# Optimization experiments

Measured on AMD Instinct MI355X. Metric: run time of the kernel, lower is better.

The kernel has to match this reference:

```python
import jax, jax.numpy as jnp
import numpy as np
from jax import lax

# Static pair index table: all C(135,2)=9045 unordered node pairs (replaces the
# nested Python loops with a single gather).
PAIR_I, PAIR_J = np.triu_indices(135, k=1)
RRELU_SLOPE = (1.0 / 8.0 + 1.0 / 3.0) / 2.0  # eval-mode RReLU negative slope
BN_SCALE = 1.0 / float(np.sqrt(1.0 + 1e-5))  # eval BN with running mean=0, var=1


def _leaky(x):
    return jnp.where(x > 0, x, 0.01 * x)


def _conv1d(x, w, b):
    # x: (N, Cin, L), w: (Cout, Cin, K) -> (N, Cout, L-K+1), VALID
    y = lax.conv_general_dilated(x, w, (1,), 'VALID',
                                 dimension_numbers=('NCH', 'OIH', 'NCH'))
    return y + b[None, :, None]


def _bn_eval(x, g, b):
    # nn.BatchNorm1d in eval with fresh running stats (mean=0, var=1)
    return x * (g * BN_SCALE)[None, :, None] + b[None, :, None]


def _maxpool2d(x):
    # nn.MaxPool2d(2) applied to a 3D (N, H, W) tensor: 2x2 pool over (H, W)
    return lax.reduce_window(x, -jnp.inf, lax.max, (1, 2, 2), (1, 2, 2), 'VALID')


def setup_inputs() -> dict:
    key = jax.random.key(0)
    ks = iter(jax.random.split(key, 40))

    def w(shape, scale=0.05):
        return (jax.random.normal(next(ks), shape, jnp.float32) * scale)

    inp = {
        'x': jax.random.normal(next(ks), (30, 135, 375), jnp.float32),
        # FeatureExtractor
        'conv1_w': w((32, 1, 3)), 'conv1_b': jnp.zeros((32,), jnp.float32),
        'bn1_g': jnp.ones((32,), jnp.float32), 'bn1_b': jnp.zeros((32,), jnp.float32),
        'conv2_w': w((64, 16, 3)), 'conv2_b': jnp.zeros((64,), jnp.float32),
        'bn2_g': jnp.ones((64,), jnp.float32), 'bn2_b': jnp.zeros((64,), jnp.float32),
        'conv3_w': w((96, 32, 3)), 'conv3_b': jnp.zeros((96,), jnp.float32),
        'bn3_g': jnp.ones((96,), jnp.float32), 'bn3_b': jnp.zeros((96,), jnp.float32),
        'fe_fc_w': w((48 * 45, 32)), 'fe_fc_b': jnp.zeros((32,), jnp.float32),
        # SimilarityMeasureNetwork
        'sim_w1': w((64, 32)), 'sim_b1': jnp.zeros((32,), jnp.float32),
        'sim_w2': w((32, 16)), 'sim_b2': jnp.zeros((16,), jnp.float32),
        'sim_w3': w((16, 8)), 'sim_b3': jnp.zeros((8,), jnp.float32),
        'sim_w4': w((8, 1)), 'sim_b4': jnp.zeros((1,), jnp.float32),
        # ClassificationNet(9045, 3)
        'cls_w1': w((9045, 1024), 0.01), 'cls_b1': jnp.zeros((1024,), jnp.float32),
        'cls_w2': w((1024, 256)), 'cls_b2': jnp.zeros((256,), jnp.float32),
        'cls_w3': w((256, 64)), 'cls_b3': jnp.zeros((64,), jnp.float32),
        'cls_w4': w((64, 3)), 'cls_b4': jnp.zeros((3,), jnp.float32),
    }
    return inp


def reference(x, conv1_w, conv1_b, bn1_g, bn1_b, conv2_w, conv2_b, bn2_g, bn2_b,
              conv3_w, conv3_b, bn3_g, bn3_b, fe_fc_w, fe_fc_b,
              sim_w1, sim_b1, sim_w2, sim_b2, sim_w3, sim_b3, sim_w4, sim_b4,
              cls_w1, cls_b1, cls_w2, cls_b2, cls_w3, cls_b3, cls_w4, cls_b4):
    B = x.shape[0]  # 30 subjects
    h = x.reshape(B * 135, 1, 375)
    # FeatureExtractor (all subjects*nodes batched together)
    h = _maxpool2d(_leaky(_bn_eval(_conv1d(h, conv1_w, conv1_b), bn1_g, bn1_b)))  # (N,16,186)
    h = _maxpool2d(_leaky(_bn_eval(_conv1d(h, conv2_w, conv2_b), bn2_g, bn2_b)))  # (N,32,92)
    h = _maxpool2d(_leaky(_bn_eval(_conv1d(h, conv3_w, conv3_b), bn3_g, bn3_b)))  # (N,48,45)
    h = h.reshape(B * 135, -1) @ fe_fc_w + fe_fc_b  # (B*135, 32)
    feats = h.reshape(B, 135, 32)

    # All-pairs concat: single gather replacing the nested loops -> (B, 9045, 64)
    pi = jnp.asarray(PAIR_I)
    pj = jnp.asarray(PAIR_J)
    pairs = jnp.concatenate([feats[:, pi, :], feats[:, pj, :]], axis=-1)

    # SimilarityMeasureNetwork
    s = jax.nn.relu(pairs @ sim_w1 + sim_b1)
    s = jax.nn.relu(s @ sim_w2 + sim_b2)
    s = jax.nn.relu(s @ sim_w3 + sim_b3)
    s = jnp.tanh(s @ sim_w4 + sim_b4)  # (B, 9045, 1)
    subjects = s[..., 0]  # (B, 9045)

    # ClassificationNet (eval mode: RReLU -> fixed slope, dropout -> identity)
    c = subjects @ cls_w1 + cls_b1
    c = jnp.where(c >= 0, c, RRELU_SLOPE * c)
    c = jax.nn.relu(c @ cls_w2 + cls_b2)
    c = jax.nn.relu(c @ cls_w3 + cls_b3)
    c = c @ cls_w4 + cls_b4
    return jax.nn.log_softmax(c, axis=1)  # (B, 3)
```

## Files before the change

kernel.cpp:

```cpp
#include <hip/hip_runtime.h>
#include <math.h>

#define BN_SCALE 0.99999500003749967f
#define RRELU_SLOPE 0.22916666666666666f

static __device__ __forceinline__ float leaky(float v) { return v > 0.f ? v : 0.01f * v; }

typedef __attribute__((ext_vector_type(8))) short bf16x8;
typedef __attribute__((ext_vector_type(4))) float f32x4;

static __device__ __forceinline__ unsigned short f2bf(float f) {
  unsigned u = __builtin_bit_cast(unsigned, f);
  u = (u + 0x7FFFu + ((u >> 16) & 1u)) >> 16;
  return (unsigned short)u;
}

__global__ __launch_bounds__(256) void prep_kernel(
    const float* __restrict__ w2c, const float* __restrict__ g2,
    const float* __restrict__ w3c, const float* __restrict__ g3,
    const float* __restrict__ fcw, const float* __restrict__ fcb,
    const float* __restrict__ w1,  const float* __restrict__ b1,
    unsigned short* __restrict__ w2frag,
    unsigned short* __restrict__ w3frag,
    unsigned short* __restrict__ bfragGG,
    float* __restrict__ bgagb,
    unsigned short* __restrict__ subjectsA)
{
  const int item = blockIdx.x * 256 + threadIdx.x;
  if (item < 512) {
    const int tile = item >> 6, lane = item & 63;
    const int mt = tile >> 1, kc = tile & 1;
    const int lr = lane & 15, quad = lane >> 4;
    const int c = mt * 16 + lr;
    const float gs = g2[c] * BN_SCALE;
#pragma unroll
    for (int j = 0; j < 8; ++j) {
      const int k = quad * 8 + j;
      float v;
      if (kc == 0) { const int tap = k >> 4, ci = k & 15; v = w2c[c * 48 + ci * 3 + tap] * gs; }
      else         { v = (k < 16) ? w2c[c * 48 + k * 3 + 2] * gs : 0.f; }
      w2frag[item * 8 + j] = f2bf(v);
    }
  } else if (item < 1664) {
    const int it = item - 512;
    const int tile = it >> 6, lane = it & 63;
    const int mt = tile / 3, tap = tile - mt * 3;
    const int lr = lane & 15, quad = lane >> 4;
    const int c = mt * 16 + lr;
    const float gs = g3[c] * BN_SCALE;
#pragma unroll
    for (int j = 0; j < 8; ++j) {
      const int ci = quad * 8 + j;
      w3frag[it * 8 + j] = f2bf(w3c[c * 96 + ci * 3 + tap] * gs);
    }
  } else if (item < 19072) {
    const int it = item - 1664;
    const int chunk = it >> 8;
    const int rem = it & 255;
    const int nt = rem >> 6;
    const int lane = rem & 63;
    const int lr = lane & 15, quad = lane >> 4;
    const int n = nt * 16 + lr;
    const int off = (n >= 32) ? 32 : 0;
    const int nj = n & 31;
    float w1col[32];
#pragma unroll 8
    for (int q = 0; q < 32; ++q) w1col[q] = w1[(q + off) * 32 + nj];
#pragma unroll
    for (int j = 0; j < 8; ++j) {
      const int k = chunk * 32 + quad * 8 + j;
      float v = 0.f;
      if (k < 2160) {
        const float* fr = fcw + (size_t)k * 32;
#pragma unroll 8
        for (int q = 0; q < 32; ++q) v = fmaf(fr[q], w1col[q], v);
      }
      bfragGG[(size_t)it * 8 + j] = f2bf(v);
    }
  } else if (item < 19136) {
    const int n = item - 19072;
    const int off = (n >= 32) ? 32 : 0;
    const int nj = n & 31;
    float s = (n < 32) ? b1[nj] : 0.f;
    for (int q = 0; q < 32; ++q) s = fmaf(fcb[q], w1[(q + off) * 32 + nj], s);
    bgagb[n] = s;
  } else if (item < 55360) {
    const int idx = item - 19136;
    uint4 z = {0u, 0u, 0u, 0u};
    ((uint4*)subjectsA)[idx] = z;
  }
}

__global__ __launch_bounds__(256) void w1t_kernel(
    const float* __restrict__ w1, unsigned short* __restrict__ w1T)
{
  __shared__ float tile[64][65];
  const int kt = blockIdx.x >> 4;
  const int ntb = blockIdx.x & 15;
  const int k0 = kt * 64, n0 = ntb * 64;
  const int t = threadIdx.x;
#pragma unroll 4
  for (int i = 0; i < 16; ++i) {
    const int idx = i * 256 + t;
    const int kk = idx >> 6, nn = idx & 63;
    const int k = k0 + kk;
    tile[kk][nn] = (k < 9045) ? w1[(size_t)k * 1024 + n0 + nn] : 0.f;
  }
  __syncthreads();
#pragma unroll 4
  for (int i = 0; i < 8; ++i) {
    const int idx = i * 256 + t;
    const int nn = idx >> 5;
    const int kp = (idx & 31) * 2;
    const unsigned lo = f2bf(tile[kp][nn]);
    const unsigned hi = f2bf(tile[kp + 1][nn]);
    ((unsigned*)w1T)[(size_t)(n0 + nn) * 4544 + (k0 >> 1) + (idx & 31)] = lo | (hi << 16);
  }
}

__global__ __launch_bounds__(128) void fe_kernel(
    const float* __restrict__ x,
    const float* __restrict__ w1c, const float* __restrict__ b1c,
    const float* __restrict__ g1,  const float* __restrict__ bb1,
    const float* __restrict__ b2c, const float* __restrict__ g2, const float* __restrict__ bb2,
    const float* __restrict__ b3c, const float* __restrict__ g3, const float* __restrict__ bb3,
    const unsigned short* __restrict__ w2frag,
    const unsigned short* __restrict__ w3frag,
    unsigned short* __restrict__ act3)
{
  __shared__ __align__(16) char smem[2 * 13120];
  const int t = threadIdx.x;
  const int wv = t >> 6, lane = t & 63, quad = lane >> 4, lr = lane & 15;
  const int n = blockIdx.x * 2 + wv;

  char* A = smem + wv * 13120;
  unsigned short* s1t = (unsigned short*)A;
  unsigned short* s2t = (unsigned short*)(A + 6208);
  float* be2 = (float*)(A + 12480);
  float* be3 = (float*)(A + 12736);

  bf16x8 a2[4][2];
#pragma unroll
  for (int mt = 0; mt < 4; ++mt)
#pragma unroll
    for (int kc = 0; kc < 2; ++kc)
      a2[mt][kc] = *(const bf16x8*)(w2frag + ((mt * 2 + kc) * 64 + lane) * 8);

  be2[lane] = b2c[lane] * (g2[lane] * BN_SCALE) + bb2[lane];
  be3[lane] = b3c[lane] * (g3[lane] * BN_SCALE) + bb3[lane];
  if (lane < 32) be3[64 + lane] = b3c[64 + lane] * (g3[64 + lane] * BN_SCALE) + bb3[64 + lane];
  ((unsigned*)s1t)[186 * 8 + lane] = 0;
  ((unsigned*)s2t)[92 * 16 + lane] = 0;
  if (lane < 32) ((unsigned*)s2t)[92 * 16 + 64 + lane] = 0;

  const int cp = lane & 7;
  float u[4][3], bbr[4];
#pragma unroll
  for (int d = 0; d < 4; ++d) {
    const int c = cp * 4 + d;
    const float gs = g1[c] * BN_SCALE;
    u[d][0] = w1c[c * 3 + 0] * gs;
    u[d][1] = w1c[c * 3 + 1] * gs;
    u[d][2] = w1c[c * 3 + 2] * gs;
    bbr[d] = b1c[c] * gs + bb1[c];
  }

  const float* xr = x + (size_t)n * 375;
  for (int o = lane; o < 1488; o += 64) {
    const int l = o >> 3;
    const int p = 2 * l;
    const float x0 = xr[p], x1 = xr[p + 1], x2 = xr[p + 2], x3 = xr[p + 3];
    unsigned pk = 0;
#pragma unroll
    for (int uu = 0; uu < 2; ++uu) {
      float m = -3.4e38f;
#pragma unroll
      for (int dc = 0; dc < 2; ++dc) {
        const int d = uu * 2 + dc;
        const float v0 = fmaf(x0, u[d][0], fmaf(x1, u[d][1], fmaf(x2, u[d][2], bbr[d])));
        const float v1 = fmaf(x1, u[d][0], fmaf(x2, u[d][1], fmaf(x3, u[d][2], bbr[d])));
        m = fmaxf(m, fmaxf(leaky(v0), leaky(v1)));
      }
      pk |= (unsigned)f2bf(m) << (16 * uu);
    }
    ((unsigned*)s1t)[l * 8 + cp] = pk;
  }

  float be2r[4][4];
#pragma unroll
  for (int mt = 0; mt < 4; ++mt)
#pragma unroll
    for (int r = 0; r < 4; ++r) be2r[mt][r] = be2[mt * 16 + quad * 4 + r];

#pragma unroll 2
  for (int nt = 0; nt < 12; ++nt) {
    const int nrow = nt * 16 + lr;
    bf16x8 b0 = *(const bf16x8*)(s1t + (nrow + (quad >> 1)) * 16 + (quad & 1) * 8);
    bf16x8 b1 = *(const bf16x8*)(s1t + (nrow + 2) * 16 + (quad & 1) * 8);
    f32x4 acc[4];
#pragma unroll
    for (int mt = 0; mt < 4; ++mt)
#pragma unroll
      for (int r = 0; r < 4; ++r) acc[mt][r] = be2r[mt][r];
#pragma unroll
    for (int mt = 0; mt < 4; ++mt)
      acc[mt] = __builtin_amdgcn_mfma_f32_16x16x32_bf16(a2[mt][0], b0, acc[mt], 0, 0, 0);
#pragma unroll
    for (int mt = 0; mt < 4; ++mt)
      acc[mt] = __builtin_amdgcn_mfma_f32_16x16x32_bf16(a2[mt][1], b1, acc[mt], 0, 0, 0);
#pragma unroll
    for (int mt = 0; mt < 4; ++mt) {
      float o[4];
#pragma unroll
      for (int r = 0; r < 4; ++r) {
        const float v = leaky(acc[mt][r]);
        o[r] = fmaxf(v, __shfl_xor(v, 1));
      }
      if ((lr & 1) == 0) {
        const int np = nrow >> 1;
        if (np <= 91) {
          const float m0 = fmaxf(o[0], o[1]);
          const float m1 = fmaxf(o[2], o[3]);
          const unsigned pk = (unsigned)f2bf(m0) | ((unsigned)f2bf(m1) << 16);
          ((unsigned*)s2t)[np * 16 + mt * 4 + quad] = pk;
        }
      }
    }
  }

  unsigned short* actr = act3 + (size_t)n * 2176;
  for (int mt = 0; mt < 6; ++mt) {
    bf16x8 a3[3];
#pragma unroll
    for (int tap = 0; tap < 3; ++tap)
      a3[tap] = *(const bf16x8*)(w3frag + ((mt * 3 + tap) * 64 + lane) * 8);
    float be3r[4];
#pragma unroll
    for (int r = 0; r < 4; ++r) be3r[r] = be3[mt * 16 + quad * 4 + r];
#pragma unroll
    for (int nt = 0; nt < 6; ++nt) {
      const int nrow = nt * 16 + lr;
      f32x4 acc;
#pragma unroll
      for (int r = 0; r < 4; ++r) acc[r] = be3r[r];
#pragma unroll
      for (int tap = 0; tap < 3; ++tap) {
        bf16x8 b = *(const bf16x8*)(s2t + (nrow + tap) * 32 + quad * 8);
        acc = __builtin_amdgcn_mfma_f32_16x16x32_bf16(a3[tap], b, acc, 0, 0, 0);
      }
      float o[4];
#pragma unroll
      for (int r = 0; r < 4; ++r) {
        const float v = leaky(acc[r]);
        o[r] = fmaxf(v, __shfl_xor(v, 1));
      }
      if ((lr & 1) == 0) {
        const int np = nrow >> 1;
        if (np <= 44) {
          const int mp = mt * 8 + quad * 2;
          actr[mp * 45 + np] = f2bf(fmaxf(o[0], o[1]));
          actr[(mp + 1) * 45 + np] = f2bf(fmaxf(o[2], o[3]));
        }
      }
    }
  }
  if (lane < 16) actr[2160 + lane] = 0;
}

__global__ __launch_bounds__(256) void gagb_kernel(
    const unsigned short* __restrict__ act3,
    const unsigned short* __restrict__ bfragGG,
    const float* __restrict__ bgagb,
    float* __restrict__ Ga, float* __restrict__ Gb)
{
  const int t = threadIdx.x;
  const int wv = t >> 6, lane = t & 63, quad = lane >> 4, lr = lane & 15;
  const int m0 = blockIdx.x * 64 + wv * 16;
  const int arow = min(m0 + lr, 4049);

  f32x4 acc[4] = {};
  for (int chunk = 0; chunk < 68; ++chunk) {
    const bf16x8 a = *(const bf16x8*)(act3 + (size_t)arow * 2176 + chunk * 32 + quad * 8);
#pragma unroll
    for (int nt = 0; nt < 4; ++nt) {
      const bf16x8 b = *(const bf16x8*)(bfragGG + ((size_t)(chunk * 4 + nt) * 64 + lane) * 8);
      acc[nt] = __builtin_amdgcn_mfma_f32_16x16x32_bf16(a, b, acc[nt], 0, 0, 0);
    }
  }
#pragma unroll
  for (int nt = 0; nt < 4; ++nt) {
    const int col = nt * 16 + lr;
    const float bias = bgagb[col];
#pragma unroll
    for (int r = 0; r < 4; ++r) {
      const int row = m0 + quad * 4 + r;
      if (row < 4050) {
        const float v = acc[nt][r] + bias;
        if (col < 32) Ga[row * 32 + col] = v;
        else          Gb[row * 32 + (col - 32)] = v;
      }
    }
  }
}

__global__ __launch_bounds__(256) void sim_kernel(
    const float* __restrict__ Ga, const float* __restrict__ Gb,
    const float* __restrict__ w2, const float* __restrict__ b2,
    const float* __restrict__ w3, const float* __restrict__ b3,
    const float* __restrict__ w4, const float* __restrict__ b4,
    unsigned short* __restrict__ subjectsA)
{
  __shared__ float sGa[135 * 36];
  __shared__ float sGb[135 * 36];
  __shared__ float sw2[512], sw3[128], sw4[8];
  __shared__ float sb2[16], sb3[8], sb4v[1];

  const int t = threadIdx.x;
  const int b = blockIdx.x >> 4;
  const int c = blockIdx.x & 15;

  for (int i = t; i < 4320; i += 256) {
    const int r = i >> 5, col = i & 31;
    sGa[r * 36 + col] = Ga[b * 4320 + i];
    sGb[r * 36 + col] = Gb[b * 4320 + i];
  }
  for (int i = t; i < 512; i += 256) sw2[i] = w2[i];
  if (t < 128) sw3[t] = w3[t];
  if (t < 8) sw4[t] = w4[t];
  if (t < 16) sb2[t] = b2[t];
  if (t < 8) sb3[t] = b3[t];
  if (t == 0) sb4v[0] = b4[0];
  __syncthreads();

  const int mtile = b >> 4, lrm = b & 15;
  const int pend = min(9045, (c + 1) * 566);
  for (int p = c * 566 + t; p < pend; p += 256) {
    int i = (int)((269.0f - sqrtf((float)(72361 - 8 * p))) * 0.5f);
    i = max(0, min(133, i));
    while (134 * (i + 1) - ((i + 1) * i) / 2 <= p) ++i;
    while (134 * i - (i * (i - 1)) / 2 > p) --i;
    const int j = i + 1 + (p - (134 * i - (i * (i - 1)) / 2));

    float h1[32];
#pragma unroll
    for (int q = 0; q < 8; ++q) {
      const float4 va = *(const float4*)(&sGa[i * 36 + 4 * q]);
      const float4 vb = *(const float4*)(&sGb[j * 36 + 4 * q]);
      h1[4 * q + 0] = fmaxf(va.x + vb.x, 0.f);
      h1[4 * q + 1] = fmaxf(va.y + vb.y, 0.f);
      h1[4 * q + 2] = fmaxf(va.z + vb.z, 0.f);
      h1[4 * q + 3] = fmaxf(va.w + vb.w, 0.f);
    }

    float h2[16];
#pragma unroll
    for (int jj = 0; jj < 16; ++jj) h2[jj] = sb2[jj];
#pragma unroll 8
    for (int ii = 0; ii < 32; ++ii) {
      const float av = h1[ii];
      const float4* wr = reinterpret_cast<const float4*>(&sw2[ii * 16]);
#pragma unroll
      for (int r = 0; r < 4; ++r) {
        float4 w = wr[r];
        h2[4 * r + 0] = fmaf(av, w.x, h2[4 * r + 0]);
        h2[4 * r + 1] = fmaf(av, w.y, h2[4 * r + 1]);
        h2[4 * r + 2] = fmaf(av, w.z, h2[4 * r + 2]);
        h2[4 * r + 3] = fmaf(av, w.w, h2[4 * r + 3]);
      }
    }
#pragma unroll
    for (int jj = 0; jj < 16; ++jj) h2[jj] = fmaxf(h2[jj], 0.f);

    float h3[8];
#pragma unroll
    for (int jj = 0; jj < 8; ++jj) h3[jj] = sb3[jj];
#pragma unroll
    for (int ii = 0; ii < 16; ++ii) {
      const float av = h2[ii];
      const float4* wr = reinterpret_cast<const float4*>(&sw3[ii * 8]);
#pragma unroll
      for (int r = 0; r < 2; ++r) {
        float4 w = wr[r];
        h3[4 * r + 0] = fmaf(av, w.x, h3[4 * r + 0]);
        h3[4 * r + 1] = fmaf(av, w.y, h3[4 * r + 1]);
        h3[4 * r + 2] = fmaf(av, w.z, h3[4 * r + 2]);
        h3[4 * r + 3] = fmaf(av, w.w, h3[4 * r + 3]);
      }
    }
#pragma unroll
    for (int jj = 0; jj < 8; ++jj) h3[jj] = fmaxf(h3[jj], 0.f);

    float z = sb4v[0];
#pragma unroll
    for (int ii = 0; ii < 8; ++ii) z = fmaf(h3[ii], sw4[ii], z);

    const float az = fabsf(z);
    const float e = __expf(-2.f * az);
    const float rr = (1.f - e) / (1.f + e);
    const float val = copysignf(rr, z);

    const int chunk = p >> 5, q8 = (p & 31) >> 3, jj2 = p & 7;
    subjectsA[chunk * 1024 + mtile * 512 + (q8 * 16 + lrm) * 8 + jj2] = f2bf(val);
  }
}

__global__ __launch_bounds__(256) void c1_kernel(
    const unsigned short* __restrict__ subjectsA,
    const unsigned short* __restrict__ w1T,
    float* __restrict__ part)
{
  const int t = threadIdx.x;
  const int wv = t >> 6, lane = t & 63, quad = lane >> 4, lr = lane & 15;
  const int job = blockIdx.x * 4 + wv;
  const int ng = job & 15;
  const int kg = job >> 4;
  const int c0 = kg * 5;
  const int cend = min(283, c0 + 5);

  f32x4 acc[2][4] = {};
  for (int ch = c0; ch < cend; ++ch) {
    const bf16x8 a0 = *(const bf16x8*)(subjectsA + ch * 1024 + lane * 8);
    const bf16x8 a1 = *(const bf16x8*)(subjectsA + ch * 1024 + 512 + lane * 8);
#pragma unroll
    for (int nt = 0; nt < 4; ++nt) {
      const int col = (ng * 4 + nt) * 16 + lr;
      const bf16x8 b = *(const bf16x8*)(w1T + (size_t)col * 9088 + ch * 32 + quad * 8);
      acc[0][nt] = __builtin_amdgcn_mfma_f32_16x16x32_bf16(a0, b, acc[0][nt], 0, 0, 0);
      acc[1][nt] = __builtin_amdgcn_mfma_f32_16x16x32_bf16(a1, b, acc[1][nt], 0, 0, 0);
    }
  }
#pragma unroll
  for (int mt = 0; mt < 2; ++mt)
#pragma unroll
    for (int r = 0; r < 4; ++r) {
      const int m = mt * 16 + quad * 4 + r;
      if (m < 30) {
#pragma unroll
        for (int nt = 0; nt < 4; ++nt) {
          const int col = (ng * 4 + nt) * 16 + lr;
          part[(size_t)(m * 64 + kg) * 1024 + col] = acc[mt][nt][r];
        }
      }
    }
}

__global__ __launch_bounds__(256) void tail_a_kernel(
    const float* __restrict__ part,
    const float* __restrict__ cb1,
    float* __restrict__ act1)
{
  const int r = blockIdx.x >> 2;
  const int cg = blockIdx.x & 3;
  const int j = cg * 256 + threadIdx.x;
  float s = cb1[j];
  const float* pp = part + (size_t)r * 64 * 1024 + j;
#pragma unroll 8
  for (int q = 0; q < 64; ++q) s += pp[q * 1024];
  act1[r * 1024 + j] = s >= 0.f ? s : RRELU_SLOPE * s;
}

__global__ __launch_bounds__(256) void tail_b_kernel(
    const float* __restrict__ act1,
    const float* __restrict__ w2, const float* __restrict__ cb2,
    float* __restrict__ act2)
{
  __shared__ float sa[1024];
  __shared__ float sp[256];
  const int r = blockIdx.x >> 3;
  const int cg = blockIdx.x & 7;
  const int t = threadIdx.x;
  const int c = t & 31;
  const int ks = t >> 5;
  const int col = cg * 32 + c;

  for (int i = t; i < 1024; i += 256) sa[i] = act1[r * 1024 + i];
  __syncthreads();

  float acc = 0.f;
  const int k0 = ks * 128;
  for (int kk = k0; kk < k0 + 128; kk += 4) {
    const float4 a = *reinterpret_cast<const float4*>(&sa[kk]);
    acc = fmaf(a.x, w2[(kk + 0) * 256 + col], acc);
    acc = fmaf(a.y, w2[(kk + 1) * 256 + col], acc);
    acc = fmaf(a.z, w2[(kk + 2) * 256 + col], acc);
    acc = fmaf(a.w, w2[(kk + 3) * 256 + col], acc);
  }
  sp[t] = acc;
  __syncthreads();
  if (t < 32) {
    float s = cb2[col];
#pragma unroll
    for (int q = 0; q < 8; ++q) s += sp[q * 32 + t];
    act2[r * 256 + cg * 32 + t] = fmaxf(s, 0.f);
  }
}

__global__ __launch_bounds__(256) void tail_c_kernel(
    const float* __restrict__ act2,
    const float* __restrict__ w3, const float* __restrict__ cb3,
    const float* __restrict__ w4, const float* __restrict__ cb4,
    float* __restrict__ out)
{
  __shared__ float sa[256];
  __shared__ float sp[256];
  __shared__ float sc3[64];
  __shared__ float slg[3];
  const int r = blockIdx.x, t = threadIdx.x;
  const int c = t & 63;
  const int ks = t >> 6;

  sa[t] = act2[r * 256 + t];
  __syncthreads();
  {
    float acc = 0.f;
    const int k0 = ks * 64;
#pragma unroll 4
    for (int kk = k0; kk < k0 + 64; ++kk)
      acc = fmaf(sa[kk], w3[kk * 64 + c], acc);
    sp[t] = acc;
  }
  __syncthreads();
  if (t < 64) {
    const float s = cb3[t] + sp[t] + sp[t + 64] + sp[t + 128] + sp[t + 192];
    sc3[t] = fmaxf(s, 0.f);
  }
  __syncthreads();
  if (t < 3) {
    float acc = cb4[t];
#pragma unroll
    for (int kk = 0; kk < 64; ++kk) acc = fmaf(sc3[kk], w4[kk * 3 + t], acc);
    slg[t] = acc;
  }
  __syncthreads();
  if (t == 0) {
    float m = fmaxf(slg[0], fmaxf(slg[1], slg[2]));
    float se = __expf(slg[0] - m) + __expf(slg[1] - m) + __expf(slg[2] - m);
    float lse = m + logf(se);
    out[r * 3 + 0] = slg[0] - lse;
    out[r * 3 + 1] = slg[1] - lse;
    out[r * 3 + 2] = slg[2] - lse;
  }
}

extern "C" void kernel_launch(void* const* d_in, const int* in_sizes, int n_in,
                              void* d_out, int out_size, void* d_ws, size_t ws_size,
                              hipStream_t stream) {
  const float* x    = (const float*)d_in[0];
  const float* w1c  = (const float*)d_in[1];
  const float* b1c  = (const float*)d_in[2];
  const float* g1   = (const float*)d_in[3];
  const float* bb1  = (const float*)d_in[4];
  const float* w2c  = (const float*)d_in[5];
  const float* b2c  = (const float*)d_in[6];
  const float* g2   = (const float*)d_in[7];
  const float* bb2  = (const float*)d_in[8];
  const float* w3c  = (const float*)d_in[9];
  const float* b3c  = (const float*)d_in[10];
  const float* g3   = (const float*)d_in[11];
  const float* bb3  = (const float*)d_in[12];
  const float* fcw  = (const float*)d_in[13];
  const float* fcb  = (const float*)d_in[14];
  const float* sw1  = (const float*)d_in[15];
  const float* sb1  = (const float*)d_in[16];
  const float* sw2  = (const float*)d_in[17];
  const float* sb2  = (const float*)d_in[18];
  const float* sw3  = (const float*)d_in[19];
  const float* sb3  = (const float*)d_in[20];
  const float* sw4  = (const float*)d_in[21];
  const float* sb4  = (const float*)d_in[22];
  const float* cw1  = (const float*)d_in[23];
  const float* cb1  = (const float*)d_in[24];
  const float* cw2  = (const float*)d_in[25];
  const float* cb2  = (const float*)d_in[26];
  const float* cw3  = (const float*)d_in[27];
  const float* cb3  = (const float*)d_in[28];
  const float* cw4  = (const float*)d_in[29];
  const float* cb4  = (const float*)d_in[30];

  float* ws = (float*)d_ws;
  float* Ga    = ws;
  float* Gb    = ws + 129600;
  float* part  = ws + 259200;
  float* bgagb = ws + 2225280;
  float* act1  = ws + 2225344;
  float* act2  = ws + 2256064;
  unsigned short* wsu = (unsigned short*)(ws + 2263744);
  unsigned short* w2frag    = wsu;
  unsigned short* w3frag    = wsu + 4096;
  unsigned short* bfragGG   = wsu + 13312;
  unsigned short* act3      = wsu + 152576;
  unsigned short* subjectsA = wsu + 8965376;
  unsigned short* w1T       = wsu + 9255168;

  prep_kernel<<<217, 256, 0, stream>>>(w2c, g2, w3c, g3, fcw, fcb, sw1, sb1,
                                       w2frag, w3frag, bfragGG, bgagb, subjectsA);
  w1t_kernel<<<2272, 256, 0, stream>>>(cw1, w1T);
  fe_kernel<<<2025, 128, 0, stream>>>(x, w1c, b1c, g1, bb1, b2c, g2, bb2,
                                      b3c, g3, bb3, w2frag, w3frag, act3);
  gagb_kernel<<<64, 256, 0, stream>>>(act3, bfragGG, bgagb, Ga, Gb);
  sim_kernel<<<480, 256, 0, stream>>>(Ga, Gb, sw2, sb2, sw3, sb3, sw4, sb4, subjectsA);
  c1_kernel<<<256, 256, 0, stream>>>(subjectsA, w1T, part);
  tail_a_kernel<<<120, 256, 0, stream>>>(part, cb1, act1);
  tail_b_kernel<<<240, 256, 0, stream>>>(act1, cw2, cb2, act2);
  tail_c_kernel<<<30, 256, 0, stream>>>(act2, cw3, cb3, cw4, cb4, (float*)d_out);
}
```

Baseline: 296.3 us.

## Merge prep kernels, alias fe LDS buffers, split-K gagb, double sim grid

Folds the w1 transpose/convert kernel into the prep kernel to save a launch. The feature-extractor reuses one LDS buffer for both stage activations, roughly halving its shared memory so more blocks fit per CU. The Ga/Gb GEMM splits K across four waves and reduces through LDS, raising the grid from 64 to 254 blocks. The similarity kernel halves its per-block pair range to launch twice as many blocks, at the cost of reloading Ga/Gb into LDS twice as often.

Measured after the change: 270.5 us. 8.7% less time.

```diff
diff --git a/kernel.cpp b/kernel.cpp
--- a/kernel.cpp
+++ b/kernel.cpp
@@ -15,21 +15,48 @@
   return (unsigned short)u;
 }
 
-__global__ __launch_bounds__(256) void prep_kernel(
+__global__ __launch_bounds__(256) void setup_kernel(
     const float* __restrict__ w2c, const float* __restrict__ g2,
     const float* __restrict__ w3c, const float* __restrict__ g3,
     const float* __restrict__ fcw, const float* __restrict__ fcb,
     const float* __restrict__ w1,  const float* __restrict__ b1,
+    const float* __restrict__ cw1,
     unsigned short* __restrict__ w2frag,
     unsigned short* __restrict__ w3frag,
     unsigned short* __restrict__ bfragGG,
     float* __restrict__ bgagb,
-    unsigned short* __restrict__ subjectsA)
-{
-  const int item = blockIdx.x * 256 + threadIdx.x;
+    unsigned short* __restrict__ subjectsA,
+    unsigned short* __restrict__ w1T)
+{
+  __shared__ float tile[64][65];
+  const int t = threadIdx.x;
+  if (blockIdx.x < 2272) {
+    const int kt = blockIdx.x >> 4;
+    const int ntb = blockIdx.x & 15;
+    const int k0 = kt * 64, n0 = ntb * 64;
+#pragma unroll 4
+    for (int i = 0; i < 16; ++i) {
+      const int idx = i * 256 + t;
+      const int kk = idx >> 6, nn = idx & 63;
+      const int k = k0 + kk;
+      tile[kk][nn] = (k < 9045) ? cw1[(size_t)k * 1024 + n0 + nn] : 0.f;
+    }
+    __syncthreads();
+#pragma unroll 4
+    for (int i = 0; i < 8; ++i) {
+      const int idx = i * 256 + t;
+      const int nn = idx >> 5;
+      const int kp = (idx & 31) * 2;
+      const unsigned lo = f2bf(tile[kp][nn]);
+      const unsigned hi = f2bf(tile[kp + 1][nn]);
+      ((unsigned*)w1T)[(size_t)(n0 + nn) * 4544 + (k0 >> 1) + (idx & 31)] = lo | (hi << 16);
+    }
+    return;
+  }
+  const int item = (blockIdx.x - 2272) * 256 + t;
   if (item < 512) {
-    const int tile = item >> 6, lane = item & 63;
-    const int mt = tile >> 1, kc = tile & 1;
+    const int tl = item >> 6, lane = item & 63;
+    const int mt = tl >> 1, kc = tl & 1;
     const int lr = lane & 15, quad = lane >> 4;
     const int c = mt * 16 + lr;
     const float gs = g2[c] * BN_SCALE;
@@ -43,8 +70,8 @@
     }
   } else if (item < 1664) {
     const int it = item - 512;
-    const int tile = it >> 6, lane = it & 63;
-    const int mt = tile / 3, tap = tile - mt * 3;
+    const int tl = it >> 6, lane = it & 63;
+    const int mt = tl / 3, tap = tl - mt * 3;
     const int lr = lane & 15, quad = lane >> 4;
     const int c = mt * 16 + lr;
     const float gs = g3[c] * BN_SCALE;
@@ -91,33 +118,6 @@
   }
 }
 
-__global__ __launch_bounds__(256) void w1t_kernel(
-    const float* __restrict__ w1, unsigned short* __restrict__ w1T)
-{
-  __shared__ float tile[64][65];
-  const int kt = blockIdx.x >> 4;
-  const int ntb = blockIdx.x & 15;
-  const int k0 = kt * 64, n0 = ntb * 64;
-  const int t = threadIdx.x;
-#pragma unroll 4
-  for (int i = 0; i < 16; ++i) {
-    const int idx = i * 256 + t;
-    const int kk = idx >> 6, nn = idx & 63;
-    const int k = k0 + kk;
-    tile[kk][nn] = (k < 9045) ? w1[(size_t)k * 1024 + n0 + nn] : 0.f;
-  }
-  __syncthreads();
-#pragma unroll 4
-  for (int i = 0; i < 8; ++i) {
-    const int idx = i * 256 + t;
-    const int nn = idx >> 5;
-    const int kp = (idx & 31) * 2;
-    const unsigned lo = f2bf(tile[kp][nn]);
-    const unsigned hi = f2bf(tile[kp + 1][nn]);
-    ((unsigned*)w1T)[(size_t)(n0 + nn) * 4544 + (k0 >> 1) + (idx & 31)] = lo | (hi << 16);
-  }
-}
-
 __global__ __launch_bounds__(128) void fe_kernel(
     const float* __restrict__ x,
     const float* __restrict__ w1c, const float* __restrict__ b1c,
@@ -128,16 +128,15 @@
     const unsigned short* __restrict__ w3frag,
     unsigned short* __restrict__ act3)
 {
-  __shared__ __align__(16) char smem[2 * 13120];
+  __shared__ __align__(16) char smem[2 * 6912];
   const int t = threadIdx.x;
   const int wv = t >> 6, lane = t & 63, quad = lane >> 4, lr = lane & 15;
   const int n = blockIdx.x * 2 + wv;
 
-  char* A = smem + wv * 13120;
-  unsigned short* s1t = (unsigned short*)A;
-  unsigned short* s2t = (unsigned short*)(A + 6208);
-  float* be2 = (float*)(A + 12480);
-  float* be3 = (float*)(A + 12736);
+  char* A = smem + wv * 6912;
+  unsigned short* buf = (unsigned short*)A;
+  float* be2 = (float*)(A + 6272);
+  float* be3 = (float*)(A + 6528);
 
   bf16x8 a2[4][2];
 #pragma unroll
@@ -149,9 +148,7 @@
   be2[lane] = b2c[lane] * (g2[lane] * BN_SCALE) + bb2[lane];
   be3[lane] = b3c[lane] * (g3[lane] * BN_SCALE) + bb3[lane];
   if (lane < 32) be3[64 + lane] = b3c[64 + lane] * (g3[64 + lane] * BN_SCALE) + bb3[64 + lane];
-  ((unsigned*)s1t)[186 * 8 + lane] = 0;
-  ((unsigned*)s2t)[92 * 16 + lane] = 0;
-  if (lane < 32) ((unsigned*)s2t)[92 * 16 + 64 + lane] = 0;
+  ((unsigned*)buf)[1488 + lane] = 0;
 
   const int cp = lane & 7;
   float u[4][3], bbr[4];
@@ -183,7 +180,7 @@
       }
       pk |= (unsigned)f2bf(m) << (16 * uu);
     }
-    ((unsigned*)s1t)[l * 8 + cp] = pk;
+    ((unsigned*)buf)[l * 8 + cp] = pk;
   }
 
   float be2r[4][4];
@@ -195,8 +192,8 @@
 #pragma unroll 2
   for (int nt = 0; nt < 12; ++nt) {
     const int nrow = nt * 16 + lr;
-    bf16x8 b0 = *(const bf16x8*)(s1t + (nrow + (quad >> 1)) * 16 + (quad & 1) * 8);
-    bf16x8 b1 = *(const bf16x8*)(s1t + (nrow + 2) * 16 + (quad & 1) * 8);
+    bf16x8 b0 = *(const bf16x8*)(buf + (nrow + (quad >> 1)) * 16 + (quad & 1) * 8);
+    bf16x8 b1 = *(const bf16x8*)(buf + (nrow + 2) * 16 + (quad & 1) * 8);
     f32x4 acc[4];
 #pragma unroll
     for (int mt = 0; mt < 4; ++mt)
@@ -222,11 +219,14 @@
           const float m0 = fmaxf(o[0], o[1]);
           const float m1 = fmaxf(o[2], o[3]);
           const unsigned pk = (unsigned)f2bf(m0) | ((unsigned)f2bf(m1) << 16);
-          ((unsigned*)s2t)[np * 16 + mt * 4 + quad] = pk;
+          ((unsigned*)buf)[np * 16 + mt * 4 + quad] = pk;
         }
       }
     }
   }
+
+  ((unsigned*)buf)[1472 + lane] = 0;
+  if (lane < 32) ((unsigned*)buf)[1536 + lane] = 0;
 
   unsigned short* actr = act3 + (size_t)n * 2176;
   for (int mt = 0; mt < 6; ++mt) {
@@ -245,7 +245,7 @@
       for (int r = 0; r < 4; ++r) acc[r] = be3r[r];
 #pragma unroll
       for (int tap = 0; tap < 3; ++tap) {
-        bf16x8 b = *(const bf16x8*)(s2t + (nrow + tap) * 32 + quad * 8);
+        bf16x8 b = *(const bf16x8*)(buf + (nrow + tap) * 32 + quad * 8);
         acc = __builtin_amdgcn_mfma_f32_16x16x32_bf16(a3[tap], b, acc, 0, 0, 0);
       }
       float o[4];
@@ -273,13 +273,15 @@
     const float* __restrict__ bgagb,
     float* __restrict__ Ga, float* __restrict__ Gb)
 {
+  __shared__ f32x4 sred[3][4][64];
   const int t = threadIdx.x;
   const int wv = t >> 6, lane = t & 63, quad = lane >> 4, lr = lane & 15;
-  const int m0 = blockIdx.x * 64 + wv * 16;
+  const int m0 = blockIdx.x * 16;
   const int arow = min(m0 + lr, 4049);
 
   f32x4 acc[4] = {};
-  for (int chunk = 0; chunk < 68; ++chunk) {
+  const int c0 = wv * 17;
+  for (int chunk = c0; chunk < c0 + 17; ++chunk) {
     const bf16x8 a = *(const bf16x8*)(act3 + (size_t)arow * 2176 + chunk * 32 + quad * 8);
 #pragma unroll
     for (int nt = 0; nt < 4; ++nt) {
@@ -287,17 +289,31 @@
       acc[nt] = __builtin_amdgcn_mfma_f32_16x16x32_bf16(a, b, acc[nt], 0, 0, 0);
     }
   }
-#pragma unroll
-  for (int nt = 0; nt < 4; ++nt) {
-    const int col = nt * 16 + lr;
-    const float bias = bgagb[col];
-#pragma unroll
-    for (int r = 0; r < 4; ++r) {
-      const int row = m0 + quad * 4 + r;
-      if (row < 4050) {
-        const float v = acc[nt][r] + bias;
-        if (col < 32) Ga[row * 32 + col] = v;
-        else          Gb[row * 32 + (col - 32)] = v;
+  if (wv > 0) {
+#pragma unroll
+    for (int nt = 0; nt < 4; ++nt) sred[wv - 1][nt][lane] = acc[nt];
+  }
+  __syncthreads();
+  if (wv == 0) {
+#pragma unroll
+    for (int nt = 0; nt < 4; ++nt) {
+      f32x4 s = acc[nt];
+#pragma unroll
+      for (int q = 0; q < 3; ++q) {
+        const f32x4 o = sred[q][nt][lane];
+#pragma unroll
+        for (int r = 0; r < 4; ++r) s[r] += o[r];
+      }
+      const int col = nt * 16 + lr;
+      const float bias = bgagb[col];
+#pragma unroll
+      for (int r = 0; r < 4; ++r) {
+        const int row = m0 + quad * 4 + r;
+        if (row < 4050) {
+          const float v = s[r] + bias;
+          if (col < 32) Ga[row * 32 + col] = v;
+          else          Gb[row * 32 + (col - 32)] = v;
+        }
       }
     }
   }
@@ -316,8 +332,8 @@
   __shared__ float sb2[16], sb3[8], sb4v[1];
 
   const int t = threadIdx.x;
-  const int b = blockIdx.x >> 4;
-  const int c = blockIdx.x & 15;
+  const int b = blockIdx.x >> 5;
+  const int c = blockIdx.x & 31;
 
   for (int i = t; i < 4320; i += 256) {
     const int r = i >> 5, col = i & 31;
@@ -333,8 +349,8 @@
   __syncthreads();
 
   const int mtile = b >> 4, lrm = b & 15;
-  const int pend = min(9045, (c + 1) * 566);
-  for (int p = c * 566 + t; p < pend; p += 256) {
+  const int pend = min(9045, (c + 1) * 283);
+  for (int p = c * 283 + t; p < pend; p += 256) {
     int i = (int)((269.0f - sqrtf((float)(72361 - 8 * p))) * 0.5f);
     i = max(0, min(133, i));
     while (134 * (i + 1) - ((i + 1) * i) / 2 <= p) ++i;
@@ -592,13 +608,12 @@
   unsigned short* subjectsA = wsu + 8965376;
   unsigned short* w1T       = wsu + 9255168;
 
-  prep_kernel<<<217, 256, 0, stream>>>(w2c, g2, w3c, g3, fcw, fcb, sw1, sb1,
-                                       w2frag, w3frag, bfragGG, bgagb, subjectsA);
-  w1t_kernel<<<2272, 256, 0, stream>>>(cw1, w1T);
+  setup_kernel<<<2489, 256, 0, stream>>>(w2c, g2, w3c, g3, fcw, fcb, sw1, sb1, cw1,
+                                         w2frag, w3frag, bfragGG, bgagb, subjectsA, w1T);
   fe_kernel<<<2025, 128, 0, stream>>>(x, w1c, b1c, g1, bb1, b2c, g2, bb2,
                                       b3c, g3, bb3, w2frag, w3frag, act3);
-  gagb_kernel<<<64, 256, 0, stream>>>(act3, bfragGG, bgagb, Ga, Gb);
-  sim_kernel<<<480, 256, 0, stream>>>(Ga, Gb, sw2, sb2, sw3, sb3, sw4, sb4, subjectsA);
+  gagb_kernel<<<254, 256, 0, stream>>>(act3, bfragGG, bgagb, Ga, Gb);
+  sim_kernel<<<960, 256, 0, stream>>>(Ga, Gb, sw2, sb2, sw3, sb3, sw4, sb4, subjectsA);
   c1_kernel<<<256, 256, 0, stream>>>(subjectsA, w1T, part);
   tail_a_kernel<<<120, 256, 0, stream>>>(part, cb1, act1);
   tail_b_kernel<<<240, 256, 0, stream>>>(act1, cw2, cb2, act2);
```
